# Kernel optimization log

Measured on AMD Instinct MI355X. Metric: run time of the kernel, lower is better.

The kernel has to match this reference:

```python
import jax, jax.numpy as jnp
import numpy as np

N, H, S = 2048, 512, 256

def setup_inputs() -> dict:
    key = jax.random.key(0)
    k1, k2, k3 = jax.random.split(key, 3)
    hidden_states = jax.random.normal(k1, (N, H, S), dtype=jnp.float32)
    # xavier_uniform-ish scale for W and context vector
    limW = float(np.sqrt(6.0 / (H + H)))
    attention_weights = jax.random.uniform(k2, (H, H), dtype=jnp.float32, minval=-limW, maxval=limW)
    attention_bias = jnp.zeros((H, 1), dtype=jnp.float32)
    limc = float(np.sqrt(6.0 / (H + 1)))
    context_vector = jax.random.uniform(k3, (H, 1), dtype=jnp.float32, minval=-limc, maxval=limc)
    return {
        "hidden_states": hidden_states,
        "attention_weights": attention_weights,
        "attention_bias": attention_bias,
        "context_vector": context_vector,
    }

def reference(hidden_states, attention_weights, attention_bias, context_vector):
    # hidden_states: (N, H, S)
    hs_t = jnp.swapaxes(hidden_states, 1, 2)              # (N, S, H)
    score = jnp.tanh(hs_t @ attention_weights + attention_bias[:, 0])  # (N, S, H)
    alignment = (score @ context_vector)[..., 0]          # (N, S)
    attn = jax.nn.softmax(alignment, axis=1)              # (N, S)
    context = jnp.einsum('ns,nhs->nh', attn, hidden_states)  # (N, H)
    return context
```

## Files before the change

### kernel.cpp

```cpp
#include <hip/hip_runtime.h>
#include <hip/hip_bf16.h>
#include <stdint.h>
#include <stddef.h>

typedef __attribute__((ext_vector_type(8))) short short8;
typedef __attribute__((ext_vector_type(4))) float f32x4;
typedef __attribute__((ext_vector_type(16))) float f32x16;

#define NB 2048
#define HD 512
#define SD 256

#define AROW 516

__device__ __forceinline__ short f2bf(float x) {
  __hip_bfloat16 h = __float2bfloat16(x);
  return *reinterpret_cast<short*>(&h);
}

__device__ __forceinline__ float fast_tanh(float x) {
  x = fminf(fmaxf(x, -15.f), 15.f);
  float e = __expf(2.f * x);
  return __fdividef(e - 1.f, e + 1.f);
}

__global__ __launch_bounds__(256) void wconv_kernel(const float* __restrict__ W,
                                                    short* __restrict__ Wtb16) {
  __shared__ float tile[32][33];
  const int bx = blockIdx.x;
  const int tk0 = (bx & 15) * 32;
  const int tj0 = (bx >> 4) * 32;
  const int lx = threadIdx.x & 31;
  const int ly = threadIdx.x >> 5;
  for (int r = 0; r < 4; ++r) {
    int yy = ly + r * 8;
    tile[yy][lx] = W[(size_t)(tk0 + yy) * HD + tj0 + lx];
  }
  __syncthreads();
  for (int r = 0; r < 4; ++r) {
    int yy = ly + r * 8;
    const int k = tk0 + lx;
    Wtb16[(size_t)(k >> 4) * (HD * 16) + (size_t)(tj0 + yy) * 16 + (k & 15)] =
        f2bf(tile[lx][yy]);
  }
}

__global__ void __launch_bounds__(512, 4)
align_kernel(const float* __restrict__ hs, const short* __restrict__ Wtb16,
             const float* __restrict__ bias, const float* __restrict__ ctxv,
             float* __restrict__ align_out)
{
  __shared__ short As[64 * AROW];
  __shared__ float abuf[64];

  const int tid = threadIdx.x;
  const int n = blockIdx.x >> 2;
  const int s0 = (blockIdx.x & 3) * 64;
  const float* hsn = hs + (size_t)n * (HD * SD) + s0;

  if (tid < 64) abuf[tid] = 0.f;

  {
    const int a_s = tid & 63;
    const int a_kg = tid >> 6;
    #pragma unroll
    for (int o = 0; o < 8; ++o) {
      const int k0 = a_kg * 64 + o * 8;
      const float* src = hsn + (size_t)k0 * SD + a_s;
      short8 pk;
      #pragma unroll
      for (int e = 0; e < 8; ++e) pk[e] = f2bf(src[(size_t)e * SD]);
      *(short8*)&As[a_s * AROW + k0] = pk;
    }
  }
  __syncthreads();

  const int lane = tid & 63;
  const int wid = tid >> 6;
  const int jb = wid * 64;
  const int l31 = lane & 31;
  const int hg = lane >> 5;

  f32x16 acc[2][2];
  #pragma unroll
  for (int i = 0; i < 2; ++i)
    #pragma unroll
    for (int p = 0; p < 2; ++p)
      #pragma unroll
      for (int q = 0; q < 16; ++q) acc[i][p][q] = 0.f;

  const short* wlane = Wtb16 + (size_t)(jb + l31) * 16 + hg * 8;
  const int afo = l31 * AROW + hg * 8;

  #pragma unroll 4
  for (int kb = 0; kb < 32; ++kb) {
    const short* wk = wlane + (size_t)kb * (HD * 16);
    short8 wf0 = *(const short8*)(wk);
    short8 wf1 = *(const short8*)(wk + 32 * 16);
    short8 af0 = *(const short8*)&As[afo + kb * 16];
    short8 af1 = *(const short8*)&As[afo + 32 * AROW + kb * 16];

    __builtin_amdgcn_s_setprio(1);
    acc[0][0] = __builtin_amdgcn_mfma_f32_32x32x16_bf16(wf0, af0, acc[0][0], 0, 0, 0);
    acc[0][1] = __builtin_amdgcn_mfma_f32_32x32x16_bf16(wf1, af0, acc[0][1], 0, 0, 0);
    acc[1][0] = __builtin_amdgcn_mfma_f32_32x32x16_bf16(wf0, af1, acc[1][0], 0, 0, 0);
    acc[1][1] = __builtin_amdgcn_mfma_f32_32x32x16_bf16(wf1, af1, acc[1][1], 0, 0, 0);
    __builtin_amdgcn_s_setprio(0);
  }

  float part0 = 0.f, part1 = 0.f;
  #pragma unroll
  for (int p = 0; p < 2; ++p) {
    const int jfr = jb + p * 32 + hg * 4;
    #pragma unroll
    for (int g = 0; g < 4; ++g) {
      const int j4 = jfr + g * 8;
      f32x4 bv = *(const f32x4*)(bias + j4);
      f32x4 cv = *(const f32x4*)(ctxv + j4);
      #pragma unroll
      for (int r = 0; r < 4; ++r) {
        const int q = g * 4 + r;
        part0 += fast_tanh(acc[0][p][q] + bv[r]) * cv[r];
        part1 += fast_tanh(acc[1][p][q] + bv[r]) * cv[r];
      }
    }
  }
  part0 += __shfl_xor(part0, 32);
  part1 += __shfl_xor(part1, 32);
  if (lane < 32) {
    atomicAdd(&abuf[l31], part0);
    atomicAdd(&abuf[32 + l31], part1);
  }
  __syncthreads();
  if (tid < 64) align_out[(size_t)n * SD + s0 + tid] = abuf[tid];
}

__global__ __launch_bounds__(256) void ctx_kernel(const float* __restrict__ hs,
                                                  const float* __restrict__ align_in,
                                                  float* __restrict__ out)
{
  __shared__ __align__(16) float attn_s[256];
  __shared__ float red[8];
  const int n = blockIdx.x;
  const int t = threadIdx.x;
  const int lane = t & 63, wid = t >> 6;

  float a = align_in[(size_t)n * 256 + t];
  float m = a;
  #pragma unroll
  for (int off = 32; off; off >>= 1) m = fmaxf(m, __shfl_xor(m, off));
  if (lane == 0) red[wid] = m;
  __syncthreads();
  m = fmaxf(fmaxf(red[0], red[1]), fmaxf(red[2], red[3]));
  float e = __expf(a - m);
  float s = e;
  #pragma unroll
  for (int off = 32; off; off >>= 1) s += __shfl_xor(s, off);
  if (lane == 0) red[4 + wid] = s;
  __syncthreads();
  s = red[4] + red[5] + red[6] + red[7];
  attn_s[t] = e / s;
  __syncthreads();

  const int grp = t & 7;
  const int hrow = t >> 3;
  float av[32];
  #pragma unroll
  for (int u = 0; u < 8; ++u) {
    float4 v = *(const float4*)&attn_s[grp * 32 + u * 4];
    av[4*u+0] = v.x; av[4*u+1] = v.y; av[4*u+2] = v.z; av[4*u+3] = v.w;
  }
  const float* hb = hs + (size_t)n * (HD * SD) + grp * 32;
  for (int it = 0; it < 16; ++it) {
    const int h = it * 32 + hrow;
    const float4* p = (const float4*)(hb + (size_t)h * SD);
    float acc = 0.f;
    #pragma unroll
    for (int u = 0; u < 8; ++u) {
      float4 v = p[u];
      acc += av[4*u+0]*v.x + av[4*u+1]*v.y + av[4*u+2]*v.z + av[4*u+3]*v.w;
    }
    acc += __shfl_xor(acc, 1);
    acc += __shfl_xor(acc, 2);
    acc += __shfl_xor(acc, 4);
    if (grp == 0) out[(size_t)n * HD + h] = acc;
  }
}

extern "C" void kernel_launch(void* const* d_in, const int* in_sizes, int n_in,
                              void* d_out, int out_size, void* d_ws, size_t ws_size,
                              hipStream_t stream) {
  (void)in_sizes; (void)n_in; (void)out_size; (void)ws_size;
  const float* hs = (const float*)d_in[0];
  const float* W  = (const float*)d_in[1];
  const float* b  = (const float*)d_in[2];
  const float* c  = (const float*)d_in[3];
  float* out = (float*)d_out;

  float* align_ws = (float*)d_ws;
  short* Wtb16 = (short*)((char*)d_ws + (size_t)NB * SD * 4);

  wconv_kernel<<<256, 256, 0, stream>>>(W, Wtb16);
  align_kernel<<<NB * 4, 512, 0, stream>>>(hs, Wtb16, b, c, align_ws);
  ctx_kernel<<<NB, 256, 0, stream>>>(hs, align_ws, out);
}
```

Measured before the change: 714.2 us.

## Shrink align tile to 32 positions, widen per-wave H span, double-buffer fragments

Each align block now handles 32 sequence positions with 256 threads, and each wave covers 128 output features (4 MFMA tiles sharing one A fragment) instead of 64x64 with 2x2 tiles. The global-to-LDS staging loads 32 strided values per thread before converting, and the MFMA loop is fully unrolled with a two-deep register prefetch of W and A fragments. This aims to raise occupancy, cut LDS use and hide load latency. In exchange, W fragments are reused across fewer positions, so each hidden_states slice causes twice as many W global reads, and register pressure goes up.

```diff
diff --git a/kernel.cpp b/kernel.cpp
--- a/kernel.cpp
+++ b/kernel.cpp
@@ -45,72 +45,93 @@
   }
 }
 
-__global__ void __launch_bounds__(512, 4)
+__global__ void __launch_bounds__(256, 4)
 align_kernel(const float* __restrict__ hs, const short* __restrict__ Wtb16,
              const float* __restrict__ bias, const float* __restrict__ ctxv,
              float* __restrict__ align_out)
 {
-  __shared__ short As[64 * AROW];
-  __shared__ float abuf[64];
+  __shared__ short As[32 * AROW];
+  __shared__ float abuf[32];
 
   const int tid = threadIdx.x;
-  const int n = blockIdx.x >> 2;
-  const int s0 = (blockIdx.x & 3) * 64;
+  const int n = blockIdx.x >> 3;
+  const int s0 = (blockIdx.x & 7) * 32;
   const float* hsn = hs + (size_t)n * (HD * SD) + s0;
 
-  if (tid < 64) abuf[tid] = 0.f;
+  if (tid < 32) abuf[tid] = 0.f;
 
   {
-    const int a_s = tid & 63;
-    const int a_kg = tid >> 6;
-    #pragma unroll
-    for (int o = 0; o < 8; ++o) {
-      const int k0 = a_kg * 64 + o * 8;
-      const float* src = hsn + (size_t)k0 * SD + a_s;
-      short8 pk;
-      #pragma unroll
-      for (int e = 0; e < 8; ++e) pk[e] = f2bf(src[(size_t)e * SD]);
-      *(short8*)&As[a_s * AROW + k0] = pk;
+    const int a_s = tid & 31;
+    const int kg = tid >> 5;
+    const float* src0 = hsn + a_s + (size_t)(kg * 64) * SD;
+    short* dst = &As[a_s * AROW + kg * 64];
+    #pragma unroll
+    for (int b = 0; b < 2; ++b) {
+      float ra[32];
+      #pragma unroll
+      for (int e = 0; e < 32; ++e)
+        ra[e] = src0[(size_t)(b * 32 + e) * SD];
+      #pragma unroll
+      for (int o = 0; o < 4; ++o) {
+        short8 pk;
+        #pragma unroll
+        for (int e = 0; e < 8; ++e) pk[e] = f2bf(ra[o * 8 + e]);
+        *(short8*)(dst + b * 32 + o * 8) = pk;
+      }
     }
   }
   __syncthreads();
 
   const int lane = tid & 63;
   const int wid = tid >> 6;
-  const int jb = wid * 64;
+  const int jb = wid * 128;
   const int l31 = lane & 31;
   const int hg = lane >> 5;
 
-  f32x16 acc[2][2];
-  #pragma unroll
-  for (int i = 0; i < 2; ++i)
-    #pragma unroll
-    for (int p = 0; p < 2; ++p)
-      #pragma unroll
-      for (int q = 0; q < 16; ++q) acc[i][p][q] = 0.f;
+  f32x16 acc[4];
+  #pragma unroll
+  for (int p = 0; p < 4; ++p)
+    #pragma unroll
+    for (int q = 0; q < 16; ++q) acc[p][q] = 0.f;
 
   const short* wlane = Wtb16 + (size_t)(jb + l31) * 16 + hg * 8;
   const int afo = l31 * AROW + hg * 8;
 
-  #pragma unroll 4
+  short8 wb[2][4];
+  short8 ab[2];
+
+  #pragma unroll
+  for (int d = 0; d < 2; ++d) {
+    const short* wk = wlane + (size_t)d * (HD * 16);
+    #pragma unroll
+    for (int p = 0; p < 4; ++p)
+      wb[d][p] = *(const short8*)(wk + p * (32 * 16));
+    ab[d] = *(const short8*)&As[afo + d * 16];
+  }
+
+  #pragma unroll
   for (int kb = 0; kb < 32; ++kb) {
-    const short* wk = wlane + (size_t)kb * (HD * 16);
-    short8 wf0 = *(const short8*)(wk);
-    short8 wf1 = *(const short8*)(wk + 32 * 16);
-    short8 af0 = *(const short8*)&As[afo + kb * 16];
-    short8 af1 = *(const short8*)&As[afo + 32 * AROW + kb * 16];
+    const int rs = kb & 1;
 
     __builtin_amdgcn_s_setprio(1);
-    acc[0][0] = __builtin_amdgcn_mfma_f32_32x32x16_bf16(wf0, af0, acc[0][0], 0, 0, 0);
-    acc[0][1] = __builtin_amdgcn_mfma_f32_32x32x16_bf16(wf1, af0, acc[0][1], 0, 0, 0);
-    acc[1][0] = __builtin_amdgcn_mfma_f32_32x32x16_bf16(wf0, af1, acc[1][0], 0, 0, 0);
-    acc[1][1] = __builtin_amdgcn_mfma_f32_32x32x16_bf16(wf1, af1, acc[1][1], 0, 0, 0);
+    acc[0] = __builtin_amdgcn_mfma_f32_32x32x16_bf16(wb[rs][0], ab[rs], acc[0], 0, 0, 0);
+    acc[1] = __builtin_amdgcn_mfma_f32_32x32x16_bf16(wb[rs][1], ab[rs], acc[1], 0, 0, 0);
+    acc[2] = __builtin_amdgcn_mfma_f32_32x32x16_bf16(wb[rs][2], ab[rs], acc[2], 0, 0, 0);
+    acc[3] = __builtin_amdgcn_mfma_f32_32x32x16_bf16(wb[rs][3], ab[rs], acc[3], 0, 0, 0);
     __builtin_amdgcn_s_setprio(0);
-  }
-
-  float part0 = 0.f, part1 = 0.f;
-  #pragma unroll
-  for (int p = 0; p < 2; ++p) {
+
+    if (kb < 30) {
+      const short* wk = wlane + (size_t)(kb + 2) * (HD * 16);
+      #pragma unroll
+      for (int p = 0; p < 4; ++p)
+        wb[rs][p] = *(const short8*)(wk + p * (32 * 16));
+      ab[rs] = *(const short8*)&As[afo + (kb + 2) * 16];
+    }
+  }
+
+  float part = 0.f;
+  #pragma unroll
+  for (int p = 0; p < 4; ++p) {
     const int jfr = jb + p * 32 + hg * 4;
     #pragma unroll
     for (int g = 0; g < 4; ++g) {
@@ -120,19 +141,14 @@
       #pragma unroll
       for (int r = 0; r < 4; ++r) {
         const int q = g * 4 + r;
-        part0 += fast_tanh(acc[0][p][q] + bv[r]) * cv[r];
-        part1 += fast_tanh(acc[1][p][q] + bv[r]) * cv[r];
+        part += fast_tanh(acc[p][q] + bv[r]) * cv[r];
       }
     }
   }
-  part0 += __shfl_xor(part0, 32);
-  part1 += __shfl_xor(part1, 32);
-  if (lane < 32) {
-    atomicAdd(&abuf[l31], part0);
-    atomicAdd(&abuf[32 + l31], part1);
-  }
-  __syncthreads();
-  if (tid < 64) align_out[(size_t)n * SD + s0 + tid] = abuf[tid];
+  part += __shfl_xor(part, 32);
+  if (lane < 32) atomicAdd(&abuf[l31], part);
+  __syncthreads();
+  if (tid < 32) align_out[(size_t)n * SD + s0 + tid] = abuf[tid];
 }
 
 __global__ __launch_bounds__(256) void ctx_kernel(const float* __restrict__ hs,
@@ -201,6 +217,6 @@
   short* Wtb16 = (short*)((char*)d_ws + (size_t)NB * SD * 4);
 
   wconv_kernel<<<256, 256, 0, stream>>>(W, Wtb16);
-  align_kernel<<<NB * 4, 512, 0, stream>>>(hs, Wtb16, b, c, align_ws);
+  align_kernel<<<NB * 8, 256, 0, stream>>>(hs, Wtb16, b, c, align_ws);
   ctx_kernel<<<NB, 256, 0, stream>>>(hs, align_ws, out);
 }
```

Measured after the change: 823.5 us. +15.3%, slower.
